# Kernel optimization log

Hardware: AMD Instinct MI355X
Metric: run time of the kernel (lower is better)

## Reference

```python
import jax, jax.numpy as jnp
import numpy as np

B, T, F, OUT = 32, 8192, 128, 1024

def setup_inputs() -> dict:
    key = jax.random.key(0)
    kx, kl = jax.random.split(key)
    x = jax.random.normal(kx, (B, T, F), dtype=jnp.float32)
    # true (unpadded) lengths; module assumes max(lengths) == T (padded length)
    lengths = jax.random.randint(kl, (B,), OUT + 1, T + 1)
    lengths = lengths.at[0].set(T)
    return {"x": x, "lengths": lengths, "output_size": OUT}

def reference(x, lengths, output_size):
    # Original math: per-sample box filter of length f_b = lengths_b - output_size + 1
    # (ones / f_b, zero-padded to max) applied as grouped conv over time:
    #   out[b, t, f] = (1/f_b) * sum_{k=0}^{f_b-1} x[b, t+k, f],  t in [0, output_size)
    # Implemented via prefix sums instead of materializing the sparse filter bank.
    fsize = lengths - output_size + 1                                  # [B]
    cs = jnp.cumsum(x, axis=1)                                         # [B, T, F]
    cs = jnp.concatenate([jnp.zeros_like(cs[:, :1]), cs], axis=1)      # [B, T+1, F]
    t = jnp.arange(output_size)                                        # [OUT]
    idx = (t[None, :] + fsize[:, None])[:, :, None]                    # [B, OUT, 1]
    hi = jnp.take_along_axis(cs, idx, axis=1)                          # [B, OUT, F]
    lo = cs[:, :output_size, :]                                        # [B, OUT, F]
    return (hi - lo) / fsize[:, None, None].astype(x.dtype)
```

## Files before the change

kernel.cpp:

```cpp
#include <hip/hip_runtime.h>

#define NB    32
#define NT    8192
#define NF    128
#define NOUT  1024
#define SEGSZ 32
#define NSEG  256
#define TILE  32
#define NTILE (NOUT/TILE)

__device__ __forceinline__ float4 f4add(float4 a, float4 b) {
  return make_float4(a.x + b.x, a.y + b.y, a.z + b.z, a.w + b.w);
}
__device__ __forceinline__ float4 f4sub(float4 a, float4 b) {
  return make_float4(a.x - b.x, a.y - b.y, a.z - b.z, a.w - b.w);
}

__global__ __launch_bounds__(256) void seg_sums(const float* __restrict__ x,
                                                const int* __restrict__ lengths,
                                                float* __restrict__ S) {
  const int blk = blockIdx.x;
  const int b   = blk >> 6;
  const int g   = blk & 63;
  const int len = lengths[b];
  if (g * 128 >= len) return;

  const int tid = threadIdx.x;
  const int f4  = tid & 31;
  const int tl  = tid >> 5;

  const float4* xp =
      reinterpret_cast<const float4*>(x + (size_t)b * NT * NF +
                                      (size_t)(g * 128) * NF) + f4;
  float4 acc = make_float4(0.f, 0.f, 0.f, 0.f);
  #pragma unroll
  for (int r = 0; r < 16; ++r)
    acc = f4add(acc, xp[(tl * 16 + r) * 32]);

  __shared__ float4 red[8][32];
  red[tl][f4] = acc;
  __syncthreads();
  if (tl < 4) {
    float4 s = f4add(red[2 * tl][f4], red[2 * tl + 1][f4]);
    reinterpret_cast<float4*>(S + ((size_t)b * NSEG + g * 4 + tl) * NF)[f4] = s;
  }
}

__global__ __launch_bounds__(256) void window_avg(const float* __restrict__ x,
                                                  const int* __restrict__ lengths,
                                                  const float* __restrict__ S,
                                                  float* __restrict__ out) {
  const int wg   = ((blockIdx.x & 7) << 7) + (blockIdx.x >> 3);
  const int b    = wg >> 5;
  const int tile = wg & (NTILE - 1);
  const int len  = lengths[b];
  const int W    = len - NOUT + 1;
  const int t0   = tile * TILE;
  const int p1   = t0 + W;
  const int s_hi = p1 >> 5;

  const int tid = threadIdx.x;
  const int f4  = tid & 31;
  const int tl  = tid >> 5;

  const float4* xb =
      reinterpret_cast<const float4*>(x + (size_t)b * NT * NF) + f4;
  const float4* Sb =
      reinterpret_cast<const float4*>(S + (size_t)b * NSEG * NF) + f4;

  float4 acc = make_float4(0.f, 0.f, 0.f, 0.f);
  for (int s = tile + tl; s < s_hi; s += 8)
    acc = f4add(acc, Sb[s * 32]);
  for (int j = (s_hi << 5) + tl; j < p1; j += 8)
    acc = f4add(acc, xb[j * 32]);

  __shared__ float4 red[8][32];
  red[tl][f4] = acc;
  __syncthreads();
  float4 A = make_float4(0.f, 0.f, 0.f, 0.f);
  #pragma unroll
  for (int k = 0; k < 8; ++k) A = f4add(A, red[k][f4]);
  __syncthreads();

  float4 D = make_float4(0.f, 0.f, 0.f, 0.f);
  if (tl < 7) {
    const int baseLo = t0 + 4 * tl;
    const int baseHi = p1 + 4 * tl;
    #pragma unroll
    for (int j = 0; j < 4; ++j) {
      float4 h = xb[(baseHi + j) * 32];
      float4 l = xb[(baseLo + j) * 32];
      D = f4add(D, f4sub(h, l));
    }
  }
  red[tl][f4] = D;
  __syncthreads();
  #pragma unroll
  for (int k = 0; k < 7; ++k)
    if (k < tl) A = f4add(A, red[k][f4]);

  const float invW  = 1.0f / (float)W;
  const int   tbase = t0 + 4 * tl;
  float4* ob =
      reinterpret_cast<float4*>(out + ((size_t)b * NOUT + tbase) * NF) + f4;

  #pragma unroll
  for (int i = 0; i < 4; ++i) {
    ob[i * 32] = make_float4(A.x * invW, A.y * invW, A.z * invW, A.w * invW);
    if (i < 3) {
      float4 h = xb[(tbase + i + W) * 32];
      float4 l = xb[(tbase + i) * 32];
      A = f4add(A, f4sub(h, l));
    }
  }
}

extern "C" void kernel_launch(void* const* d_in, const int* in_sizes, int n_in,
                              void* d_out, int out_size, void* d_ws, size_t ws_size,
                              hipStream_t stream) {
  const float* x       = (const float*)d_in[0];
  const int*   lengths = (const int*)d_in[1];
  float*       S       = (float*)d_ws;
  float*       out     = (float*)d_out;

  hipLaunchKernelGGL(seg_sums, dim3(NB * 64), dim3(256), 0, stream,
                     x, lengths, S);
  hipLaunchKernelGGL(window_avg, dim3(NB * NTILE), dim3(256), 0, stream,
                     x, lengths, S, out);
}
```

Baseline: 32.05 us.

## Fuse segment-sum and window passes into one cooperative kernel with grid sync

Merges the two launches into a single cooperative kernel. Each block first computes segment sums for four 128-row groups, then waits at a grid-wide barrier, then computes a 64-row output tile. It also adds a coarser 128-row sum level so the window prefix needs fewer loads. Tiles double from 32 to 64 outputs, so each thread handles 8 rows instead of 4. This targets the launch gap between kernels and the prefix-load cost, at the price of grid-sync overhead, fewer blocks (512) and an added fallback path.

```diff
diff --git a/kernel.cpp b/kernel.cpp
--- a/kernel.cpp
+++ b/kernel.cpp
@@ -1,13 +1,17 @@
 #include <hip/hip_runtime.h>
+#include <hip/hip_cooperative_groups.h>
+
+namespace cg = cooperative_groups;
 
 #define NB    32
 #define NT    8192
 #define NF    128
 #define NOUT  1024
-#define SEGSZ 32
 #define NSEG  256
-#define TILE  32
-#define NTILE (NOUT/TILE)
+#define NGRP  64
+#define TILE  64
+#define NTILE 16
+#define GRID  (NB * NTILE)
 
 __device__ __forceinline__ float4 f4add(float4 a, float4 b) {
   return make_float4(a.x + b.x, a.y + b.y, a.z + b.z, a.w + b.w);
@@ -16,98 +20,95 @@
   return make_float4(a.x - b.x, a.y - b.y, a.z - b.z, a.w - b.w);
 }
 
-__global__ __launch_bounds__(256) void seg_sums(const float* __restrict__ x,
-                                                const int* __restrict__ lengths,
-                                                float* __restrict__ S) {
-  const int blk = blockIdx.x;
-  const int b   = blk >> 6;
-  const int g   = blk & 63;
-  const int len = lengths[b];
-  if (g * 128 >= len) return;
-
-  const int tid = threadIdx.x;
-  const int f4  = tid & 31;
-  const int tl  = tid >> 5;
-
-  const float4* xp =
-      reinterpret_cast<const float4*>(x + (size_t)b * NT * NF +
-                                      (size_t)(g * 128) * NF) + f4;
-  float4 acc = make_float4(0.f, 0.f, 0.f, 0.f);
-  #pragma unroll
-  for (int r = 0; r < 16; ++r)
-    acc = f4add(acc, xp[(tl * 16 + r) * 32]);
-
-  __shared__ float4 red[8][32];
-  red[tl][f4] = acc;
-  __syncthreads();
-  if (tl < 4) {
-    float4 s = f4add(red[2 * tl][f4], red[2 * tl + 1][f4]);
-    reinterpret_cast<float4*>(S + ((size_t)b * NSEG + g * 4 + tl) * NF)[f4] = s;
+__device__ __forceinline__ void phase1_group(const float4* __restrict__ xb,
+                                             int b, int gg, int len,
+                                             float* __restrict__ S32,
+                                             float* __restrict__ S128,
+                                             int tl, int fl, float4 (*red)[32]) {
+  if (gg * 128 < len) {
+    const float4* xp = xb + (size_t)(gg * 128) * 32;
+    float4 acc = make_float4(0.f, 0.f, 0.f, 0.f);
+    #pragma unroll
+    for (int r = 0; r < 16; ++r)
+      acc = f4add(acc, xp[(tl * 16 + r) * 32]);
+    red[tl][fl] = acc;
+    __syncthreads();
+    if (tl < 4) {
+      float4 s = f4add(red[2 * tl][fl], red[2 * tl + 1][fl]);
+      reinterpret_cast<float4*>(S32 + ((size_t)b * NSEG + gg * 4 + tl) * NF)[fl] = s;
+    } else if (tl == 4) {
+      float4 s = f4add(f4add(red[0][fl], red[1][fl]),
+                       f4add(red[2][fl], red[3][fl]));
+      s = f4add(s, f4add(f4add(red[4][fl], red[5][fl]),
+                         f4add(red[6][fl], red[7][fl])));
+      reinterpret_cast<float4*>(S128 + ((size_t)b * NGRP + gg) * NF)[fl] = s;
+    }
+    __syncthreads();
   }
 }
 
-__global__ __launch_bounds__(256) void window_avg(const float* __restrict__ x,
-                                                  const int* __restrict__ lengths,
-                                                  const float* __restrict__ S,
-                                                  float* __restrict__ out) {
-  const int wg   = ((blockIdx.x & 7) << 7) + (blockIdx.x >> 3);
-  const int b    = wg >> 5;
-  const int tile = wg & (NTILE - 1);
-  const int len  = lengths[b];
+__device__ __forceinline__ void phase2_tile(const float4* __restrict__ xb,
+                                            int b, int tile, int len,
+                                            const float* __restrict__ S32,
+                                            const float* __restrict__ S128,
+                                            float* __restrict__ out,
+                                            int tl, int fl, float4 (*red)[32]) {
   const int W    = len - NOUT + 1;
   const int t0   = tile * TILE;
   const int p1   = t0 + W;
+  const int s_lo = t0 >> 5;
   const int s_hi = p1 >> 5;
+  const int g_lo = (t0 + 127) >> 7;
+  const int g_hi = p1 >> 7;
 
-  const int tid = threadIdx.x;
-  const int f4  = tid & 31;
-  const int tl  = tid >> 5;
-
-  const float4* xb =
-      reinterpret_cast<const float4*>(x + (size_t)b * NT * NF) + f4;
-  const float4* Sb =
-      reinterpret_cast<const float4*>(S + (size_t)b * NSEG * NF) + f4;
+  const float4* S32b  = reinterpret_cast<const float4*>(S32  + (size_t)b * NSEG * NF) + fl;
+  const float4* S128b = reinterpret_cast<const float4*>(S128 + (size_t)b * NGRP * NF) + fl;
 
   float4 acc = make_float4(0.f, 0.f, 0.f, 0.f);
-  for (int s = tile + tl; s < s_hi; s += 8)
-    acc = f4add(acc, Sb[s * 32]);
+  if (g_hi > g_lo) {
+    for (int s = s_lo + tl; s < 4 * g_lo; s += 8)
+      acc = f4add(acc, S32b[s * 32]);
+    for (int g = g_lo + tl; g < g_hi; g += 8)
+      acc = f4add(acc, S128b[g * 32]);
+    for (int s = 4 * g_hi + tl; s < s_hi; s += 8)
+      acc = f4add(acc, S32b[s * 32]);
+  } else {
+    for (int s = s_lo + tl; s < s_hi; s += 8)
+      acc = f4add(acc, S32b[s * 32]);
+  }
   for (int j = (s_hi << 5) + tl; j < p1; j += 8)
     acc = f4add(acc, xb[j * 32]);
 
-  __shared__ float4 red[8][32];
-  red[tl][f4] = acc;
+  red[tl][fl] = acc;
   __syncthreads();
   float4 A = make_float4(0.f, 0.f, 0.f, 0.f);
   #pragma unroll
-  for (int k = 0; k < 8; ++k) A = f4add(A, red[k][f4]);
+  for (int k = 0; k < 8; ++k) A = f4add(A, red[k][fl]);
   __syncthreads();
 
   float4 D = make_float4(0.f, 0.f, 0.f, 0.f);
   if (tl < 7) {
-    const int baseLo = t0 + 4 * tl;
-    const int baseHi = p1 + 4 * tl;
+    const int baseLo = t0 + 8 * tl;
+    const int baseHi = p1 + 8 * tl;
     #pragma unroll
-    for (int j = 0; j < 4; ++j) {
-      float4 h = xb[(baseHi + j) * 32];
-      float4 l = xb[(baseLo + j) * 32];
-      D = f4add(D, f4sub(h, l));
-    }
+    for (int j = 0; j < 8; ++j)
+      D = f4add(D, f4sub(xb[(baseHi + j) * 32], xb[(baseLo + j) * 32]));
   }
-  red[tl][f4] = D;
+  red[tl][fl] = D;
   __syncthreads();
   #pragma unroll
   for (int k = 0; k < 7; ++k)
-    if (k < tl) A = f4add(A, red[k][f4]);
+    if (k < tl) A = f4add(A, red[k][fl]);
 
   const float invW  = 1.0f / (float)W;
-  const int   tbase = t0 + 4 * tl;
+  const int   tbase = t0 + 8 * tl;
   float4* ob =
-      reinterpret_cast<float4*>(out + ((size_t)b * NOUT + tbase) * NF) + f4;
+      reinterpret_cast<float4*>(out + ((size_t)b * NOUT + tbase) * NF) + fl;
 
   #pragma unroll
-  for (int i = 0; i < 4; ++i) {
+  for (int i = 0; i < 8; ++i) {
     ob[i * 32] = make_float4(A.x * invW, A.y * invW, A.z * invW, A.w * invW);
-    if (i < 3) {
+    if (i < 7) {
       float4 h = xb[(tbase + i + W) * 32];
       float4 l = xb[(tbase + i) * 32];
       A = f4add(A, f4sub(h, l));
@@ -115,16 +116,83 @@
   }
 }
 
+__global__ __launch_bounds__(256, 2) void fused(const float* __restrict__ x,
+                                                const int* __restrict__ lengths,
+                                                float* __restrict__ S32,
+                                                float* __restrict__ S128,
+                                                float* __restrict__ out) {
+  const int bid = blockIdx.x;
+  const int wg  = ((bid & 7) << 6) + (bid >> 3);
+  const int b   = wg >> 4;
+  const int sub = wg & 15;
+  const int len = lengths[b];
+  const int tid = threadIdx.x;
+  const int fl  = tid & 31;
+  const int tl  = tid >> 5;
+
+  __shared__ float4 red[8][32];
+  const float4* xb = reinterpret_cast<const float4*>(x + (size_t)b * NT * NF) + fl;
+
+  #pragma unroll
+  for (int q = 0; q < 4; ++q)
+    phase1_group(xb, b, sub * 4 + q, len, S32, S128, tl, fl, red);
+
+  cg::this_grid().sync();
+
+  phase2_tile(xb, b, sub, len, S32, S128, out, tl, fl, red);
+}
+
+__global__ __launch_bounds__(256) void k_seg(const float* __restrict__ x,
+                                             const int* __restrict__ lengths,
+                                             float* __restrict__ S32,
+                                             float* __restrict__ S128) {
+  const int blk = blockIdx.x;
+  const int b   = blk >> 6;
+  const int gg  = blk & 63;
+  const int len = lengths[b];
+  const int tid = threadIdx.x;
+  const int fl  = tid & 31;
+  const int tl  = tid >> 5;
+  __shared__ float4 red[8][32];
+  const float4* xb = reinterpret_cast<const float4*>(x + (size_t)b * NT * NF) + fl;
+  phase1_group(xb, b, gg, len, S32, S128, tl, fl, red);
+}
+
+__global__ __launch_bounds__(256) void k_win(const float* __restrict__ x,
+                                             const int* __restrict__ lengths,
+                                             const float* __restrict__ S32,
+                                             const float* __restrict__ S128,
+                                             float* __restrict__ out) {
+  const int bid = blockIdx.x;
+  const int wg  = ((bid & 7) << 6) + (bid >> 3);
+  const int b   = wg >> 4;
+  const int tile = wg & 15;
+  const int len = lengths[b];
+  const int tid = threadIdx.x;
+  const int fl  = tid & 31;
+  const int tl  = tid >> 5;
+  __shared__ float4 red[8][32];
+  const float4* xb = reinterpret_cast<const float4*>(x + (size_t)b * NT * NF) + fl;
+  phase2_tile(xb, b, tile, len, S32, S128, out, tl, fl, red);
+}
+
 extern "C" void kernel_launch(void* const* d_in, const int* in_sizes, int n_in,
                               void* d_out, int out_size, void* d_ws, size_t ws_size,
                               hipStream_t stream) {
   const float* x       = (const float*)d_in[0];
   const int*   lengths = (const int*)d_in[1];
-  float*       S       = (float*)d_ws;
+  float*       S32     = (float*)d_ws;
+  float*       S128    = (float*)d_ws + (size_t)NB * NSEG * NF;
   float*       out     = (float*)d_out;
 
-  hipLaunchKernelGGL(seg_sums, dim3(NB * 64), dim3(256), 0, stream,
-                     x, lengths, S);
-  hipLaunchKernelGGL(window_avg, dim3(NB * NTILE), dim3(256), 0, stream,
-                     x, lengths, S, out);
+  void* args[] = {(void*)&x, (void*)&lengths, (void*)&S32, (void*)&S128, (void*)&out};
+  hipError_t e = hipLaunchCooperativeKernel((void*)fused, dim3(GRID), dim3(256),
+                                            args, 0, stream);
+  if (e != hipSuccess) {
+    (void)hipGetLastError();
+    hipLaunchKernelGGL(k_seg, dim3(NB * NGRP), dim3(256), 0, stream,
+                       x, lengths, S32, S128);
+    hipLaunchKernelGGL(k_win, dim3(GRID), dim3(256), 0, stream,
+                       x, lengths, S32, S128, out);
+  }
 }
```

New measurement: 97.65 us. 3.05x slower.
